# Kernel tuning notes

Hardware: AMD Instinct MI355X
Metric: run time of the kernel (lower is better)

## Reference

```python
import jax, jax.numpy as jnp
import numpy as np

H = 16      # num heads
DH = 64     # head dim
D = H * DH  # hidden = 1024

def setup_inputs() -> dict:
    key = jax.random.key(0)
    ks = jax.random.split(key, 8)
    B, S = 4, 2048
    scale = 1.0 / np.sqrt(D)
    return {
        "hidden_states": jax.random.normal(ks[0], (B, S, D), dtype=jnp.float32),
        "attention_mask": jnp.zeros((B, S, S), dtype=jnp.float32),
        "Wq": jax.random.normal(ks[1], (D, D), dtype=jnp.float32) * scale,
        "bq": jnp.zeros((D,), dtype=jnp.float32),
        "Wk": jax.random.normal(ks[2], (D, D), dtype=jnp.float32) * scale,
        "bk": jnp.zeros((D,), dtype=jnp.float32),
        "Wv": jax.random.normal(ks[3], (D, D), dtype=jnp.float32) * scale,
        "bv": jnp.zeros((D,), dtype=jnp.float32),
    }

def _split_heads(x):
    B, S, _ = x.shape
    return x.reshape(B, S, H, DH).transpose(0, 2, 1, 3)  # [B,H,S,dh]

def reference(hidden_states, attention_mask, Wq, bq, Wk, bk, Wv, bv):
    q = _split_heads(hidden_states @ Wq + bq)
    k = _split_heads(hidden_states @ Wk + bk)
    v = _split_heads(hidden_states @ Wv + bv)
    scores = jnp.einsum("bhqd,bhkd->bhqk", q, k) / jnp.sqrt(jnp.float32(DH))
    scores = scores + attention_mask[:, None, :, :]
    probs = jax.nn.softmax(scores, axis=-1)  # dropout p=0 (eval) -> identity
    ctx = jnp.einsum("bhqk,bhkd->bhqd", probs, v)
    B, _, S, _ = ctx.shape
    return ctx.transpose(0, 2, 1, 3).reshape(B, S, H * DH)
```

## Files before the change

### kernel.cpp

```cpp
#include <hip/hip_runtime.h>

typedef __bf16 bf16;
typedef __bf16 bf16x8 __attribute__((ext_vector_type(8)));
typedef __bf16 bf16x4 __attribute__((ext_vector_type(4)));
typedef float floatx4 __attribute__((ext_vector_type(4)));
typedef float floatx16 __attribute__((ext_vector_type(16)));
typedef unsigned int uint4t __attribute__((ext_vector_type(4)));

typedef __attribute__((address_space(1))) void gvoid;
typedef __attribute__((address_space(3))) void lvoid;
#define ASYNC_COPY16(gp, lp) \
  __builtin_amdgcn_global_load_lds((gvoid*)(gp), (lvoid*)(lp), 16, 0, 0)

#define NB 4
#define SQ 2048
#define DMODEL 1024
#define NH 16
#define HD 64
#define MTOK (NB * SQ)
#define LOG2E 1.44269504088896f

#define XB_OFF 0ull
#define WT_OFF (16ull * 1024 * 1024)
#define Q_OFF  (22ull * 1024 * 1024)
#define K_OFF  (38ull * 1024 * 1024)
#define V_OFF  (54ull * 1024 * 1024)
#define FLG_OFF (70ull * 1024 * 1024)

__global__ __launch_bounds__(256) void prep(
    const float* __restrict__ x, bf16* __restrict__ xb,
    const float* __restrict__ w0, const float* __restrict__ w1,
    const float* __restrict__ w2, bf16* __restrict__ wt,
    const float* __restrict__ mask, int* __restrict__ flags) {
  __shared__ float t4[4][32][33];
  int blk = blockIdx.x;
  int t = threadIdx.x;
  if (blk < 1024) {
    size_t base = (size_t)blk * 2048 + t;
    const float4* xin = (const float4*)x;
    bf16x4* xo = (bf16x4*)xb;
#pragma unroll
    for (int j = 0; j < 8; j++) {
      float4 v = xin[base + j * 256];
      bf16x4 o;
      o[0] = (bf16)v.x; o[1] = (bf16)v.y; o[2] = (bf16)v.z; o[3] = (bf16)v.w;
      xo[base + j * 256] = o;
    }
  } else if (blk < 1792) {
    int tidx = blk - 1024;
    int z = tidx >> 8;
    int rem = tidx & 255;
    int kbase = (rem >> 5) * 128;
    int nb = (rem & 31) * 32;
    const float* w = (z == 0) ? w0 : (z == 1) ? w1 : w2;
    bf16* out = wt + (size_t)z * DMODEL * DMODEL;
    int tx = t & 31, ty = t >> 5;
#pragma unroll
    for (int i4 = 0; i4 < 4; i4++) {
      int kb = kbase + i4 * 32;
#pragma unroll
      for (int i = 0; i < 4; i++)
        t4[i4][ty + 8 * i][tx] = w[(size_t)(kb + ty + 8 * i) * DMODEL + nb + tx];
    }
    __syncthreads();
#pragma unroll
    for (int i4 = 0; i4 < 4; i4++) {
      int kb = kbase + i4 * 32;
#pragma unroll
      for (int i = 0; i < 4; i++)
        out[(size_t)(nb + ty + 8 * i) * DMODEL + kb + tx] = (bf16)t4[i4][tx][ty + 8 * i];
    }
  } else {
    int midx = blk - 1792;
    int kt = midx & 31, qt = (midx >> 5) & 15, b = midx >> 9;
    const float* mb = mask + ((size_t)b * SQ + qt * 128) * SQ + kt * 64;
    int row = t >> 1, half = t & 1;
    const float4* p = (const float4*)(mb + (size_t)row * SQ + half * 32);
    bool nz = false;
#pragma unroll
    for (int i = 0; i < 8; i++) {
      float4 vv = p[i];
      nz |= (vv.x != 0.f) | (vv.y != 0.f) | (vv.z != 0.f) | (vv.w != 0.f);
    }
    int* acc = (int*)t4;
    if (t == 0) acc[0] = 0;
    __syncthreads();
    unsigned long long m = __ballot(nz);
    if ((t & 63) == 0 && m) atomicOr(acc, 1);
    __syncthreads();
    if (t == 0) flags[(b * 16 + qt) * 32 + kt] = acc[0];
  }
}

#define BK 64
__global__ __launch_bounds__(256) void qkv(
    const bf16* __restrict__ xb,
    const bf16* __restrict__ wt,
    const float* __restrict__ biasq, const float* __restrict__ biask,
    const float* __restrict__ biasv,
    bf16* __restrict__ q, bf16* __restrict__ k, bf16* __restrict__ v) {
  __shared__ bf16 smem[2 * 128 * BK];
  bf16* As = smem;
  bf16* Bs = smem + 128 * BK;

  int id = blockIdx.x;
  int local = id >> 3;
  int mt = ((id & 7) << 3) | (local & 7);
  int nt = local >> 3;
  int t = threadIdx.x;

  int mat = nt >> 3;
  int nbase = (nt & 7) * 128;
  const bf16* wmat = wt + (size_t)mat * DMODEL * DMODEL;
  const float* bias = (mat == 0) ? biasq : (mat == 1) ? biask : biasv;
  bf16* outp = (mat == 0) ? q : (mat == 1) ? k : v;

  int lane = t & 63, wid = t >> 6;
  int quad = lane >> 4, l16 = lane & 15;
  int wm = (wid & 1) * 64, wn = (wid >> 1) * 64;
  int xq = quad ^ (l16 & 7);

  floatx4 acc[4][4] = {};

  for (int kb = 0; kb < DMODEL; kb += BK) {
    __syncthreads();
#pragma unroll
    for (int p = 0; p < 4; p++) {
      int i2 = p * 256 + t;
      int row = i2 >> 3;
      int gch = (i2 ^ row) & 7;
      ASYNC_COPY16(xb + (size_t)(mt * 128 + row) * DMODEL + kb + gch * 8,
                   As + i2 * 8);
      ASYNC_COPY16(wmat + (size_t)(nbase + row) * DMODEL + kb + gch * 8,
                   Bs + i2 * 8);
    }
    __syncthreads();

#pragma unroll
    for (int kc = 0; kc < BK; kc += 32) {
      int xc = (kc >> 3) ^ xq;
      bf16x8 af[4], bfr[4];
#pragma unroll
      for (int mi = 0; mi < 4; mi++)
        af[mi] = *(const bf16x8*)(As + (wm + mi * 16 + l16) * BK + xc * 8);
#pragma unroll
      for (int ni = 0; ni < 4; ni++)
        bfr[ni] = *(const bf16x8*)(Bs + (wn + ni * 16 + l16) * BK + xc * 8);
      if (mat < 2) {
#pragma unroll
        for (int mi = 0; mi < 4; mi++)
#pragma unroll
          for (int ni = 0; ni < 4; ni++)
            acc[mi][ni] = __builtin_amdgcn_mfma_f32_16x16x32_bf16(
                bfr[ni], af[mi], acc[mi][ni], 0, 0, 0);
      } else {
#pragma unroll
        for (int mi = 0; mi < 4; mi++)
#pragma unroll
          for (int ni = 0; ni < 4; ni++)
            acc[mi][ni] = __builtin_amdgcn_mfma_f32_16x16x32_bf16(
                af[mi], bfr[ni], acc[mi][ni], 0, 0, 0);
      }
    }
  }

  int mg0 = mt * 128 + wm;
  if (mat < 2) {
    float qscale = (mat == 0) ? 0.125f * LOG2E : 1.0f;
    __syncthreads();
#pragma unroll
    for (int ni = 0; ni < 4; ni++) {
      int n0 = nbase + wn + ni * 16 + quad * 4;
      float4 bv4 = *(const float4*)(bias + n0);
      int nc = wn + ni * 16 + quad * 4;
      int unit = nc >> 3, h8 = (nc >> 2) & 1;
#pragma unroll
      for (int mi = 0; mi < 4; mi++) {
        int sr = wm + mi * 16 + l16;
        bf16x4 pk;
        pk[0] = (bf16)((acc[mi][ni][0] + bv4.x) * qscale);
        pk[1] = (bf16)((acc[mi][ni][1] + bv4.y) * qscale);
        pk[2] = (bf16)((acc[mi][ni][2] + bv4.z) * qscale);
        pk[3] = (bf16)((acc[mi][ni][3] + bv4.w) * qscale);
        int su = unit ^ (sr & 15);
        *(bf16x4*)(smem + sr * 128 + su * 8 + h8 * 4) = pk;
      }
    }
    __syncthreads();
    int sr = t >> 1, half = t & 1;
    int bb = mt >> 4;
    int s = ((mt & 15) << 7) + sr;
    int h = (nbase >> 6) + half;
    bf16* gout = outp + (((size_t)(bb * NH + h) * SQ + s) << 6);
#pragma unroll
    for (int i = 0; i < 8; i++) {
      int su = (half * 8 + i) ^ (sr & 15);
      bf16x8 ch = *(const bf16x8*)(smem + sr * 128 + su * 8);
      *(bf16x8*)(gout + i * 8) = ch;
    }
  } else {
#pragma unroll
    for (int ni = 0; ni < 4; ni++) {
      int n = nbase + wn + ni * 16 + l16;
      int h = n >> 6, d = n & 63;
      float bv_ = bias[n];
#pragma unroll
      for (int mi = 0; mi < 4; mi++) {
        int m0 = mg0 + mi * 16 + quad * 4;
        int b = m0 >> 11, s = m0 & 2047;
        bf16x4 pk;
#pragma unroll
        for (int r = 0; r < 4; r++) pk[r] = (bf16)(acc[mi][ni][r] + bv_);
        *(bf16x4*)(outp + (((size_t)(b * NH + h) * HD + d) << 11) + s) = pk;
      }
    }
  }
}

__global__ __launch_bounds__(256, 4) void attn(
    const bf16* __restrict__ Q,
    const bf16* __restrict__ K,
    const bf16* __restrict__ Vt,
    const float* __restrict__ mask,
    const int* __restrict__ flags,
    float* __restrict__ out) {
  __shared__ bf16 Ks[64 * 64];
  __shared__ bf16 Vs[64 * 64];

  int bh = blockIdx.x;
  int qt = blockIdx.y;
  int b = bh >> 4, h = bh & 15;
  int t = threadIdx.x, lane = t & 63, wid = t >> 6;
  int l32 = lane & 31, hi = lane >> 5;
  int q0 = qt * 128 + wid * 32;

  const bf16* Qp = Q + ((size_t)bh * SQ + q0) * HD;
  const bf16* Kp = K + (size_t)bh * SQ * HD;
  const bf16* Vp = Vt + (size_t)bh * HD * SQ;
  const float* mp = mask + ((size_t)b * SQ + q0) * SQ;
  const int* flg = flags + (b * 16 + qt) * 32;

  bf16x8 qa[4];
#pragma unroll
  for (int dp = 0; dp < 4; dp++)
    qa[dp] = *(const bf16x8*)(Qp + (size_t)l32 * HD + dp * 16 + hi * 8);

  floatx16 o2[2] = {};
  float li = 0.f;

  for (int kb = 0, kti = 0; kb < SQ; kb += 64, kti++) {
    __syncthreads();
#pragma unroll
    for (int p = 0; p < 2; p++) {
      int idx = p * 256 + t;
      int row = idx >> 3;
      int gch = (idx ^ row) & 7;
      ASYNC_COPY16(Kp + (size_t)(kb + row) * HD + gch * 8, Ks + idx * 8);
      ASYNC_COPY16(Vp + (size_t)row * SQ + kb + gch * 8, Vs + idx * 8);
    }
    __syncthreads();
    int flag = flg[kti];

    bf16x8 pf[2][2];
#pragma unroll
    for (int kt = 0; kt < 2; kt++) {
      int row = kt * 32 + l32;
      const bf16* kr = Ks + row * 64;
      floatx16 z = {};
      __builtin_amdgcn_s_setprio(1);
#pragma unroll
      for (int dp = 0; dp < 4; dp++) {
        int ch = (dp * 2 + hi) ^ (row & 7);
        bf16x8 kf = *(const bf16x8*)(kr + ch * 8);
        z = __builtin_amdgcn_mfma_f32_32x32x16_bf16(kf, qa[dp], z, 0, 0, 0);
      }
      __builtin_amdgcn_s_setprio(0);
      if (flag) {
#pragma unroll
        for (int r = 0; r < 16; r++) {
          int kk = kb + kt * 32 + (r & 3) + 8 * (r >> 2) + 4 * hi;
          z[r] = __builtin_fmaf(mp[(size_t)l32 * SQ + kk], LOG2E, z[r]);
        }
      }
      float e[16];
      float s = 0.f;
#pragma unroll
      for (int r = 0; r < 16; r++) {
        e[r] = __builtin_amdgcn_exp2f(z[r]);
        s += e[r];
      }
      li += s;
#pragma unroll
      for (int kp = 0; kp < 2; kp++) {
        int bs = kp * 8;
        unsigned int u0, u1, u2, u3;
        asm("v_cvt_pk_bf16_f32 %0, %1, %2" : "=v"(u0) : "v"(e[bs + 0]), "v"(e[bs + 1]));
        asm("v_cvt_pk_bf16_f32 %0, %1, %2" : "=v"(u1) : "v"(e[bs + 2]), "v"(e[bs + 3]));
        asm("v_cvt_pk_bf16_f32 %0, %1, %2" : "=v"(u2) : "v"(e[bs + 4]), "v"(e[bs + 5]));
        asm("v_cvt_pk_bf16_f32 %0, %1, %2" : "=v"(u3) : "v"(e[bs + 6]), "v"(e[bs + 7]));
        asm("v_permlane32_swap_b32 %0, %1" : "+v"(u0), "+v"(u2));
        asm("v_permlane32_swap_b32 %0, %1" : "+v"(u1), "+v"(u3));
        uint4t w;
        w[0] = u0; w[1] = u1; w[2] = u2; w[3] = u3;
        pf[kt][kp] = __builtin_bit_cast(bf16x8, w);
      }
    }

    __builtin_amdgcn_s_setprio(1);
#pragma unroll
    for (int dt = 0; dt < 2; dt++) {
      int row = dt * 32 + l32;
      const bf16* vr = Vs + row * 64;
#pragma unroll
      for (int kt = 0; kt < 2; kt++)
#pragma unroll
        for (int kp = 0; kp < 2; kp++) {
          int ch = (kt * 4 + kp * 2 + hi) ^ (row & 7);
          bf16x8 vf = *(const bf16x8*)(vr + ch * 8);
          o2[dt] = __builtin_amdgcn_mfma_f32_32x32x16_bf16(vf, pf[kt][kp], o2[dt], 0, 0, 0);
        }
    }
    __builtin_amdgcn_s_setprio(0);
  }

  li += __shfl_xor(li, 32, 64);
  float inv = 1.0f / li;
  float* op = out + ((size_t)b * SQ + q0 + l32) * DMODEL + h * HD;
#pragma unroll
  for (int dt = 0; dt < 2; dt++)
#pragma unroll
    for (int g = 0; g < 4; g++) {
      float4 w;
      w.x = o2[dt][g * 4 + 0] * inv;
      w.y = o2[dt][g * 4 + 1] * inv;
      w.z = o2[dt][g * 4 + 2] * inv;
      w.w = o2[dt][g * 4 + 3] * inv;
      *(float4*)(op + dt * 32 + g * 8 + hi * 4) = w;
    }
}

extern "C" void kernel_launch(void* const* d_in, const int* in_sizes, int n_in,
                              void* d_out, int out_size, void* d_ws, size_t ws_size,
                              hipStream_t stream) {
  (void)in_sizes; (void)n_in; (void)out_size; (void)ws_size;
  const float* hs   = (const float*)d_in[0];
  const float* mask = (const float*)d_in[1];
  const float* Wq   = (const float*)d_in[2];
  const float* bq   = (const float*)d_in[3];
  const float* Wk   = (const float*)d_in[4];
  const float* bk   = (const float*)d_in[5];
  const float* Wv   = (const float*)d_in[6];
  const float* bv   = (const float*)d_in[7];
  float* out = (float*)d_out;
  char* ws = (char*)d_ws;
  bf16* xb = (bf16*)(ws + XB_OFF);
  bf16* wt = (bf16*)(ws + WT_OFF);
  bf16* q  = (bf16*)(ws + Q_OFF);
  bf16* k  = (bf16*)(ws + K_OFF);
  bf16* v  = (bf16*)(ws + V_OFF);
  int* flg = (int*)(ws + FLG_OFF);

  prep<<<1024 + 768 + 2048, 256, 0, stream>>>(hs, xb, Wq, Wk, Wv, wt, mask, flg);
  qkv<<<1536, 256, 0, stream>>>(xb, wt, bq, bk, bv, q, k, v);
  attn<<<dim3(64, 16), 256, 0, stream>>>(q, k, v, mask, flg, out);
}
```

Measured before the change: 299.0 us.

## Double-buffer QKV GEMM loads and widen tiles to 128x256 with 512 threads

Restructures the QKV projection GEMM so each 512-thread block computes a 128x256 output tile. The block-index decode and epilogue smem layout are adjusted to match, and half the blocks are launched. K-step loads are double-buffered with async global-to-LDS copies, so the next stage is issued before computing on the current one, using explicit vmcnt waits and barriers. This aims to hide global-load latency and raise A-tile reuse, at the cost of 96KB of LDS (one block per CU) and fewer total blocks.

```diff
diff --git a/kernel.cpp b/kernel.cpp
--- a/kernel.cpp
+++ b/kernel.cpp
@@ -93,15 +93,13 @@
 }
 
 #define BK 64
-__global__ __launch_bounds__(256) void qkv(
+__global__ __launch_bounds__(512, 1) void qkv(
     const bf16* __restrict__ xb,
     const bf16* __restrict__ wt,
     const float* __restrict__ biasq, const float* __restrict__ biask,
     const float* __restrict__ biasv,
     bf16* __restrict__ q, bf16* __restrict__ k, bf16* __restrict__ v) {
-  __shared__ bf16 smem[2 * 128 * BK];
-  bf16* As = smem;
-  bf16* Bs = smem + 128 * BK;
+  __shared__ bf16 smem[49152];
 
   int id = blockIdx.x;
   int local = id >> 3;
@@ -109,33 +107,56 @@
   int nt = local >> 3;
   int t = threadIdx.x;
 
-  int mat = nt >> 3;
-  int nbase = (nt & 7) * 128;
+  int mat = nt >> 2;
+  int nbase = (nt & 3) * 256;
   const bf16* wmat = wt + (size_t)mat * DMODEL * DMODEL;
   const float* bias = (mat == 0) ? biasq : (mat == 1) ? biask : biasv;
   bf16* outp = (mat == 0) ? q : (mat == 1) ? k : v;
 
   int lane = t & 63, wid = t >> 6;
   int quad = lane >> 4, l16 = lane & 15;
-  int wm = (wid & 1) * 64, wn = (wid >> 1) * 64;
+  int wm = (wid & 1) * 64;
+  int wn = (wid >> 1) * 64;
   int xq = quad ^ (l16 & 7);
 
   floatx4 acc[4][4] = {};
 
-  for (int kb = 0; kb < DMODEL; kb += BK) {
-    __syncthreads();
+  auto STAGE = [&](int ks, int d) {
+    int kb = ks * BK;
+    bf16* Ad = smem + d * 8192;
+    bf16* Bd = smem + 16384 + d * 16384;
+#pragma unroll
+    for (int p = 0; p < 2; p++) {
+      int idx = p * 512 + t;
+      int row = idx >> 3;
+      int gch = (idx ^ row) & 7;
+      ASYNC_COPY16(xb + (size_t)(mt * 128 + row) * DMODEL + kb + gch * 8,
+                   Ad + idx * 8);
+    }
 #pragma unroll
     for (int p = 0; p < 4; p++) {
-      int i2 = p * 256 + t;
-      int row = i2 >> 3;
-      int gch = (i2 ^ row) & 7;
-      ASYNC_COPY16(xb + (size_t)(mt * 128 + row) * DMODEL + kb + gch * 8,
-                   As + i2 * 8);
+      int idx = p * 512 + t;
+      int row = idx >> 3;
+      int gch = (idx ^ row) & 7;
       ASYNC_COPY16(wmat + (size_t)(nbase + row) * DMODEL + kb + gch * 8,
-                   Bs + i2 * 8);
-    }
-    __syncthreads();
-
+                   Bd + idx * 8);
+    }
+  };
+
+  STAGE(0, 0);
+  for (int ks = 0; ks < 16; ks++) {
+    int cur = ks & 1;
+    if (ks < 15) {
+      STAGE(ks + 1, cur ^ 1);
+      asm volatile("s_waitcnt vmcnt(6)" ::: "memory");
+    } else {
+      asm volatile("s_waitcnt vmcnt(0)" ::: "memory");
+    }
+    __builtin_amdgcn_s_barrier();
+    __builtin_amdgcn_sched_barrier(0);
+
+    const bf16* As = smem + cur * 8192;
+    const bf16* Bs = smem + 16384 + cur * 16384;
 #pragma unroll
     for (int kc = 0; kc < BK; kc += 32) {
       int xc = (kc >> 3) ^ xq;
@@ -162,6 +183,8 @@
                 af[mi], bfr[ni], acc[mi][ni], 0, 0, 0);
       }
     }
+    __builtin_amdgcn_s_barrier();
+    __builtin_amdgcn_sched_barrier(0);
   }
 
   int mg0 = mt * 128 + wm;
@@ -170,9 +193,8 @@
     __syncthreads();
 #pragma unroll
     for (int ni = 0; ni < 4; ni++) {
-      int n0 = nbase + wn + ni * 16 + quad * 4;
-      float4 bv4 = *(const float4*)(bias + n0);
       int nc = wn + ni * 16 + quad * 4;
+      float4 bv4 = *(const float4*)(bias + nbase + nc);
       int unit = nc >> 3, h8 = (nc >> 2) & 1;
 #pragma unroll
       for (int mi = 0; mi < 4; mi++) {
@@ -182,20 +204,20 @@
         pk[1] = (bf16)((acc[mi][ni][1] + bv4.y) * qscale);
         pk[2] = (bf16)((acc[mi][ni][2] + bv4.z) * qscale);
         pk[3] = (bf16)((acc[mi][ni][3] + bv4.w) * qscale);
-        int su = unit ^ (sr & 15);
-        *(bf16x4*)(smem + sr * 128 + su * 8 + h8 * 4) = pk;
-      }
-    }
-    __syncthreads();
-    int sr = t >> 1, half = t & 1;
+        int su = unit ^ (sr & 31);
+        *(bf16x4*)(smem + sr * 256 + su * 8 + h8 * 4) = pk;
+      }
+    }
+    __syncthreads();
+    int sr = t >> 2, seg = t & 3;
     int bb = mt >> 4;
     int s = ((mt & 15) << 7) + sr;
-    int h = (nbase >> 6) + half;
+    int h = (nbase >> 6) + seg;
     bf16* gout = outp + (((size_t)(bb * NH + h) * SQ + s) << 6);
 #pragma unroll
     for (int i = 0; i < 8; i++) {
-      int su = (half * 8 + i) ^ (sr & 15);
-      bf16x8 ch = *(const bf16x8*)(smem + sr * 128 + su * 8);
+      int su = (seg * 8 + i) ^ (sr & 31);
+      bf16x8 ch = *(const bf16x8*)(smem + sr * 256 + su * 8);
       *(bf16x8*)(gout + i * 8) = ch;
     }
   } else {
@@ -361,6 +383,6 @@
   int* flg = (int*)(ws + FLG_OFF);
 
   prep<<<1024 + 768 + 2048, 256, 0, stream>>>(hs, xb, Wq, Wk, Wv, wt, mask, flg);
-  qkv<<<1536, 256, 0, stream>>>(xb, wt, bq, bk, bv, q, k, v);
+  qkv<<<768, 512, 0, stream>>>(xb, wt, bq, bk, bv, q, k, v);
   attn<<<dim3(64, 16), 256, 0, stream>>>(q, k, v, mask, flg, out);
 }
```

Result: no change. 301.0 us (+0.7%).
